# Optimization experiments

Measured on AMD Instinct MI355X. Metric: run time of the kernel, lower is better.

The kernel has to match this reference:

```python
import math
import jax, jax.numpy as jnp
import numpy as np

B, T, E = 1, 4096, 768
H, D = 12, 64
RA_WINDOW = 512
INIT_GATES = (2.2, 0.6, 0.1)


def setup_inputs() -> dict:
    key = jax.random.key(0)
    ks = jax.random.split(key, 6)
    x = jax.random.normal(ks[0], (B, T, E), dtype=jnp.float32)
    # Linear weights stored as [in, out] (math-equivalent to torch's x @ W.T)
    s = 1.0 / math.sqrt(E)
    Wq = jax.random.normal(ks[1], (E, H * D), dtype=jnp.float32) * s
    Wk = jax.random.normal(ks[2], (E, H * D), dtype=jnp.float32) * s
    Wv = jax.random.normal(ks[3], (E, H * D), dtype=jnp.float32) * s
    Wo = jax.random.normal(ks[4], (H * D, E), dtype=jnp.float32) * s
    gates = jnp.tile(jnp.asarray(INIT_GATES, dtype=jnp.float32)[None, :], (H, 1))  # [H,3]
    u = jax.random.normal(ks[5], (H, D), dtype=jnp.float32) * 0.02
    return {"x": x, "Wq": Wq, "Wk": Wk, "Wv": Wv, "Wo": Wo, "gates": gates, "u": u}


def reference(x, Wq, Wk, Wv, Wo, gates, u):
    # projections -> [B,H,T,D]
    def proj(W):
        return (x @ W).reshape(B, T, H, D).transpose(0, 2, 1, 3)
    Q, K, V = proj(Wq), proj(Wk), proj(Wv)

    S = jnp.einsum('bhtd,bhsd->bhts', Q, K) / math.sqrt(D)  # [B,H,T,T]

    w = jax.nn.softmax(gates, axis=-1)  # [H,3]
    w_std = w[:, 0][None, :, None, None]
    w_rec = w[:, 1][None, :, None, None]
    w_disc = w[:, 2][None, :, None, None]

    logits = w_std * S + w_rec * jnp.swapaxes(S, -2, -1)

    # discoverability column bias from K via per-head u
    d_raw = jnp.einsum('bhtd,hd->bht', K, u)
    d = d_raw - jnp.mean(d_raw, axis=-1, keepdims=True)
    logits = logits + w_disc * d[:, :, None, :]

    # causal banded mask
    idx = jnp.arange(T)
    mask = (idx[None, :] <= idx[:, None]) & (jnp.abs(idx[None, :] - idx[:, None]) <= RA_WINDOW)
    logits = jnp.where(mask[None, None, :, :], logits, -jnp.inf)

    attn = jax.nn.softmax(logits, axis=-1)
    ctx = jnp.einsum('bhts,bhsd->bhtd', attn, V)
    out = ctx.transpose(0, 2, 1, 3).reshape(B, T, H * D) @ Wo
    return (out, attn)
```

## Files before the change

kernel.cpp:

```cpp
#include <hip/hip_runtime.h>
#include <cstddef>

#define T_LEN 4096
#define EMB 768
#define NH 12
#define HD 64
#define WIN 512
#define PBW 640

#define GBM 128
#define GBN 128
#define GBK 16

__device__ __forceinline__ void gemm_128(const float* __restrict__ A,
                                         const float* __restrict__ B,
                                         float* __restrict__ C,
                                         int bm, int bn, int tid) {
    __shared__ float As[GBK][GBM + 4];
    __shared__ float Bs[GBK][GBN + 4];

    const int ty = (tid >> 4) << 2;
    const int tx = (tid & 15) << 2;

    const int ar = tid >> 1;
    const int ac = (tid & 1) << 3;
    const int br = tid >> 4;
    const int bc = (tid & 15) << 3;

    float acc[8][8] = {};

    float4 pa0 = *(const float4*)&A[(size_t)(bm + ar) * EMB + ac];
    float4 pa1 = *(const float4*)&A[(size_t)(bm + ar) * EMB + ac + 4];
    float4 pb0 = *(const float4*)&B[(size_t)br * EMB + bn + bc];
    float4 pb1 = *(const float4*)&B[(size_t)br * EMB + bn + bc + 4];

    for (int k0 = 0; k0 < EMB; k0 += GBK) {
        As[ac + 0][ar] = pa0.x; As[ac + 1][ar] = pa0.y; As[ac + 2][ar] = pa0.z; As[ac + 3][ar] = pa0.w;
        As[ac + 4][ar] = pa1.x; As[ac + 5][ar] = pa1.y; As[ac + 6][ar] = pa1.z; As[ac + 7][ar] = pa1.w;
        *(float4*)&Bs[br][bc]     = pb0;
        *(float4*)&Bs[br][bc + 4] = pb1;
        __syncthreads();
        if (k0 + GBK < EMB) {
            pa0 = *(const float4*)&A[(size_t)(bm + ar) * EMB + k0 + GBK + ac];
            pa1 = *(const float4*)&A[(size_t)(bm + ar) * EMB + k0 + GBK + ac + 4];
            pb0 = *(const float4*)&B[(size_t)(k0 + GBK + br) * EMB + bn + bc];
            pb1 = *(const float4*)&B[(size_t)(k0 + GBK + br) * EMB + bn + bc + 4];
        }
#pragma unroll
        for (int k = 0; k < GBK; ++k) {
            const float4 a0v = *(const float4*)&As[k][ty];
            const float4 a1v = *(const float4*)&As[k][ty + 64];
            const float4 b0v = *(const float4*)&Bs[k][tx];
            const float4 b1v = *(const float4*)&Bs[k][tx + 64];
            const float av[8] = {a0v.x, a0v.y, a0v.z, a0v.w, a1v.x, a1v.y, a1v.z, a1v.w};
            const float bv[8] = {b0v.x, b0v.y, b0v.z, b0v.w, b1v.x, b1v.y, b1v.z, b1v.w};
#pragma unroll
            for (int i = 0; i < 8; ++i)
#pragma unroll
                for (int j = 0; j < 8; ++j)
                    acc[i][j] += av[i] * bv[j];
        }
        __syncthreads();
    }
#pragma unroll
    for (int i = 0; i < 8; ++i) {
        const int r = bm + ty + ((i < 4) ? i : (60 + i));
        *(float4*)&C[(size_t)r * EMB + bn + tx]      = make_float4(acc[i][0], acc[i][1], acc[i][2], acc[i][3]);
        *(float4*)&C[(size_t)r * EMB + bn + tx + 64] = make_float4(acc[i][4], acc[i][5], acc[i][6], acc[i][7]);
    }
}

__global__ __launch_bounds__(256) void qkv_zero_kernel(const float* __restrict__ x,
                                                       const float* __restrict__ Wq,
                                                       const float* __restrict__ Wk,
                                                       const float* __restrict__ Wv,
                                                       float* __restrict__ Qb,
                                                       float* __restrict__ Kb,
                                                       float* __restrict__ Vb,
                                                       float* __restrict__ attn) {
    const int bid = blockIdx.x;
    const int tid = threadIdx.x;
    if (bid < 576) {
        const int z = bid / 192;
        const int r = bid % 192;
        const int bm = (r / 6) * GBM;
        const int bn = (r % 6) * GBN;
        const float* B = (z == 0) ? Wq : (z == 1) ? Wk : Wv;
        float* C = (z == 0) ? Qb : (z == 1) ? Kb : Vb;
        gemm_128(x, B, C, bm, bn, tid);
    } else {
        const int zb = bid - 576;
        const int rr0 = tid >> 6;
        const int ln = tid & 63;
        const float4 z4 = make_float4(0.f, 0.f, 0.f, 0.f);
        for (int k = 0; k < 4; ++k) {
            const int p = zb + 192 * k;
            const int h = p % NH;
            const int t0 = (p / NH) << 6;
            const int bl = (t0 >= 576) ? (t0 - 576) : 0;
            const int br = t0 + 64;
            for (int rr = rr0; rr < 64; rr += 4) {
                float* arow = attn + ((size_t)(h * T_LEN + t0 + rr)) * T_LEN;
                for (int c = ln << 2; c < bl; c += 256)
                    *(float4*)&arow[c] = z4;
                for (int c = br + (ln << 2); c < T_LEN; c += 256)
                    *(float4*)&arow[c] = z4;
            }
        }
    }
}

__global__ __launch_bounds__(256) void dbias_kernel(const float* __restrict__ K,
                                                    const float* __restrict__ u,
                                                    float* __restrict__ d_bias) {
    const int h = blockIdx.x;
    const int tid = threadIdx.x;
    __shared__ __align__(16) float us[HD];
    __shared__ float dr[T_LEN];
    __shared__ float red[256];
    if (tid < HD) us[tid] = u[h * HD + tid];
    __syncthreads();
    const float4* u4 = (const float4*)us;
    float lsum = 0.f;
    for (int t = tid; t < T_LEN; t += 256) {
        const float4* Kp = (const float4*)&K[(size_t)t * EMB + h * HD];
        float acc = 0.f;
#pragma unroll
        for (int i = 0; i < HD / 4; ++i) {
            float4 k4 = Kp[i];
            float4 uu = u4[i];
            acc += k4.x * uu.x + k4.y * uu.y + k4.z * uu.z + k4.w * uu.w;
        }
        dr[t] = acc;
        lsum += acc;
    }
    red[tid] = lsum;
    __syncthreads();
    for (int off = 128; off > 0; off >>= 1) {
        if (tid < off) red[tid] += red[tid + off];
        __syncthreads();
    }
    const float mean = red[0] * (1.0f / (float)T_LEN);
    __syncthreads();
    for (int t = tid; t < T_LEN; t += 256) {
        d_bias[h * T_LEN + t] = dr[t] - mean;
    }
}

__global__ __launch_bounds__(256) void attn_band_kernel(const float* __restrict__ Q,
                                                        const float* __restrict__ K,
                                                        const float* __restrict__ V,
                                                        const float* __restrict__ d_bias,
                                                        const float* __restrict__ gates,
                                                        float* __restrict__ Pb,
                                                        float* __restrict__ Fb,
                                                        float* __restrict__ ctx) {
    const int t0  = blockIdx.x << 6;
    const int h   = blockIdx.y;
    const int tid = threadIdx.x;
    const int cg  = tid & 15;
    const int tm  = (tid >> 4) << 2;
    const int tn4 = cg << 2;

    const int lm = tid >> 2;
    const int lk = (tid & 3) << 4;
    const int sr = tid >> 1;
    const int sc = (tid & 1) << 5;

    __shared__ __align__(16) float QT[64][68];
    __shared__ __align__(16) float KT[64][68];
    __shared__ __align__(16) float Bc[64][136];
    __shared__ float cmf[5][64];
    __shared__ float rmf[64], idvf[64];
    float* __restrict__ Bp = &Bc[0][0];

    const float g0 = gates[h * 3 + 0];
    const float g1 = gates[h * 3 + 1];
    const float g2 = gates[h * 3 + 2];
    const float gm = fmaxf(g0, fmaxf(g1, g2));
    const float e0 = __expf(g0 - gm), e1 = __expf(g1 - gm), e2 = __expf(g2 - gm);
    const float gi = 1.0f / (e0 + e1 + e2);
    const float w_std = e0 * gi * 0.125f;
    const float w_rec = e1 * gi * 0.125f;
    const float w_disc = e2 * gi;

    const int cp_start = (t0 >= 576) ? 0 : ((576 - t0) >> 7);
    int s0 = t0 - 576 + (cp_start << 7);

    float4 kr[8], qr[8];
    {
        int srow = s0 + sr; srow = srow < 0 ? 0 : srow;
        const float* Kp = K + (size_t)srow * EMB + h * HD + sc;
#pragma unroll
        for (int c = 0; c < 8; ++c) kr[c] = *(const float4*)(Kp + 4 * c);
    }

    {
        const float* Qp = Q + (size_t)(t0 + lm) * EMB + h * HD + lk;
        const float* Kp = K + (size_t)(t0 + lm) * EMB + h * HD + lk;
#pragma unroll
        for (int it = 0; it < 4; ++it) {
            float4 a = *(const float4*)(Qp + 4 * it);
            QT[lk + 4 * it + 0][lm] = a.x;
            QT[lk + 4 * it + 1][lm] = a.y;
            QT[lk + 4 * it + 2][lm] = a.z;
            QT[lk + 4 * it + 3][lm] = a.w;
            float4 b = *(const float4*)(Kp + 4 * it);
            KT[lk + 4 * it + 0][lm] = b.x;
            KT[lk + 4 * it + 1][lm] = b.y;
            KT[lk + 4 * it + 2][lm] = b.z;
            KT[lk + 4 * it + 3][lm] = b.w;
        }
    }

    float rm[4], rden[4], acc[4][4];
#pragma unroll
    for (int i = 0; i < 4; ++i) {
        rm[i] = -1e30f;
        rden[i] = 0.f;
#pragma unroll
        for (int j = 0; j < 4; ++j) acc[i][j] = 0.f;
    }

    for (int cp = cp_start; cp < 5; ++cp) {
        __syncthreads();
#pragma unroll
        for (int c = 0; c < 8; ++c) {
            Bc[sc + 4 * c + 0][sr] = kr[c].x;
            Bc[sc + 4 * c + 1][sr] = kr[c].y;
            Bc[sc + 4 * c + 2][sr] = kr[c].z;
            Bc[sc + 4 * c + 3][sr] = kr[c].w;
        }
        __syncthreads();

        {
            int srow = s0 + sr; srow = srow < 0 ? 0 : srow;
            const float* Qp = Q + (size_t)srow * EMB + h * HD + sc;
#pragma unroll
            for (int c = 0; c < 8; ++c) qr[c] = *(const float4*)(Qp + 4 * c);
        }

        float m1[4][8] = {};
#pragma unroll 8
        for (int k = 0; k < 64; ++k) {
            const float4 a4 = *(const float4*)&QT[k][tm];
            const float4 b0 = *(const float4*)&Bc[k][tn4];
            const float4 b1 = *(const float4*)&Bc[k][tn4 + 64];
            const float av[4] = {a4.x, a4.y, a4.z, a4.w};
            const float bv[8] = {b0.x, b0.y, b0.z, b0.w, b1.x, b1.y, b1.z, b1.w};
#pragma unroll
            for (int i = 0; i < 4; ++i)
#pragma unroll
                for (int j = 0; j < 8; ++j)
                    m1[i][j] += av[i] * bv[j];
        }
        __syncthreads();

#pragma unroll
        for (int c = 0; c < 8; ++c) {
            Bc[sc + 4 * c + 0][sr] = qr[c].x;
            Bc[sc + 4 * c + 1][sr] = qr[c].y;
            Bc[sc + 4 * c + 2][sr] = qr[c].z;
            Bc[sc + 4 * c + 3][sr] = qr[c].w;
        }
        __syncthreads();

        if (cp < 4) {
            int srow = s0 + 128 + sr; srow = srow < 0 ? 0 : srow;
            const float* Kp = K + (size_t)srow * EMB + h * HD + sc;
#pragma unroll
            for (int c = 0; c < 8; ++c) kr[c] = *(const float4*)(Kp + 4 * c);
        }

        float m2[4][8] = {};
#pragma unroll 8
        for (int k = 0; k < 64; ++k) {
            const float4 a4 = *(const float4*)&KT[k][tm];
            const float4 b0 = *(const float4*)&Bc[k][tn4];
            const float4 b1 = *(const float4*)&Bc[k][tn4 + 64];
            const float av[4] = {a4.x, a4.y, a4.z, a4.w};
            const float bv[8] = {b0.x, b0.y, b0.z, b0.w, b1.x, b1.y, b1.z, b1.w};
#pragma unroll
            for (int i = 0; i < 4; ++i)
#pragma unroll
                for (int j = 0; j < 8; ++j)
                    m2[i][j] += av[i] * bv[j];
        }

        const int i0 = s0 + tn4;
        const int i0c = i0 < 0 ? 0 : i0;
        const float4 db0 = *(const float4*)&d_bias[h * T_LEN + i0c];
        const float4 db1 = *(const float4*)&d_bias[h * T_LEN + s0 + 64 + tn4];
        const float dbv[8] = {db0.x, db0.y, db0.z, db0.w, db1.x, db1.y, db1.z, db1.w};
        float l[4][8];
#pragma unroll
        for (int i = 0; i < 4; ++i) {
            const int t = t0 + tm + i;
#pragma unroll
            for (int j = 0; j < 8; ++j) {
                const int s = s0 + ((j < 4) ? (tn4 + j) : (tn4 + j + 60));
                const float lv = w_std * m1[i][j] + w_rec * m2[i][j] + w_disc * dbv[j];
                const bool valid = (s >= 0) && (s <= t) && (s >= t - WIN);
                l[i][j] = valid ? lv : -1e30f;
            }
        }
#pragma unroll
        for (int i = 0; i < 4; ++i) {
            float cmx = fmaxf(fmaxf(fmaxf(l[i][0], l[i][1]), fmaxf(l[i][2], l[i][3])),
                              fmaxf(fmaxf(l[i][4], l[i][5]), fmaxf(l[i][6], l[i][7])));
#pragma unroll
            for (int off = 1; off < 16; off <<= 1) cmx = fmaxf(cmx, __shfl_xor(cmx, off));
            const float nm = fmaxf(rm[i], cmx);
            const float f = __expf(rm[i] - nm);
            float cs = 0.f;
#pragma unroll
            for (int j = 0; j < 8; ++j) {
                const float p = __expf(l[i][j] - nm);
                l[i][j] = p;
                cs += p;
            }
#pragma unroll
            for (int off = 1; off < 16; off <<= 1) cs += __shfl_xor(cs, off);
            rden[i] = rden[i] * f + cs;
            rm[i] = nm;
#pragma unroll
            for (int j = 0; j < 4; ++j) acc[i][j] *= f;
            if (cg == 0) cmf[cp][tm + i] = nm;
            float* prow = &Pb[((size_t)(h * T_LEN + t0 + tm + i)) * PBW + (cp << 7)];
            *(float4*)&prow[tn4]      = make_float4(l[i][0], l[i][1], l[i][2], l[i][3]);
            *(float4*)&prow[64 + tn4] = make_float4(l[i][4], l[i][5], l[i][6], l[i][7]);
        }
        __syncthreads();

#pragma unroll
        for (int j = 0; j < 4; ++j) {
            *(float4*)&Bp[(tn4 + j) * 68 + tm] =
                make_float4(l[0][j], l[1][j], l[2][j], l[3][j]);
            *(float4*)&Bp[(tn4 + j + 64) * 68 + tm] =
                make_float4(l[0][j + 4], l[1][j + 4], l[2][j + 4], l[3][j + 4]);
        }
        __syncthreads();

#pragma unroll 8
        for (int k = 0; k < 128; ++k) {
            const float4 av = *(const float4*)&Bp[k * 68 + tm];
            int vrow = s0 + k; vrow = vrow < 0 ? 0 : vrow;
            const float4 bv = *(const float4*)&V[(size_t)vrow * EMB + h * HD + tn4];
            acc[0][0] += av.x * bv.x; acc[0][1] += av.x * bv.y; acc[0][2] += av.x * bv.z; acc[0][3] += av.x * bv.w;
            acc[1][0] += av.y * bv.x; acc[1][1] += av.y * bv.y; acc[1][2] += av.y * bv.z; acc[1][3] += av.y * bv.w;
            acc[2][0] += av.z * bv.x; acc[2][1] += av.z * bv.y; acc[2][2] += av.z * bv.z; acc[2][3] += av.z * bv.w;
            acc[3][0] += av.w * bv.x; acc[3][1] += av.w * bv.y; acc[3][2] += av.w * bv.z; acc[3][3] += av.w * bv.w;
        }
        s0 += 128;
    }

    float idv[4];
#pragma unroll
    for (int i = 0; i < 4; ++i) {
        idv[i] = 1.0f / rden[i];
        *(float4*)&ctx[(size_t)(t0 + tm + i) * EMB + h * HD + tn4] =
            make_float4(acc[i][0] * idv[i], acc[i][1] * idv[i], acc[i][2] * idv[i], acc[i][3] * idv[i]);
    }
    if (cg == 0) {
#pragma unroll
        for (int i = 0; i < 4; ++i) {
            rmf[tm + i] = rm[i];
            idvf[tm + i] = idv[i];
        }
    }
    __syncthreads();
    for (int idx = tid; idx < 320; idx += 256) {
        const int c = idx >> 6, r = idx & 63;
        const float fct = (c >= cp_start) ? __expf(cmf[c][r] - rmf[r]) * idvf[r] : 0.f;
        Fb[((size_t)(h * T_LEN + t0 + r)) * 5 + c] = fct;
    }
}

__global__ __launch_bounds__(256) void wo_expand_kernel(const float* __restrict__ Cb,
                                                        const float* __restrict__ Wo,
                                                        float* __restrict__ out,
                                                        const float* __restrict__ Pb,
                                                        const float* __restrict__ Fb,
                                                        float* __restrict__ attn) {
    const int bid = blockIdx.x;
    const int tid = threadIdx.x;
    if (bid < 192) {
        const int bm = (bid / 6) * GBM;
        const int bn = (bid % 6) * GBN;
        gemm_128(Cb, Wo, out, bm, bn, tid);
    } else {
        const int e = bid - 192;
        const int h = e / 1024;
        const int t = ((e % 1024) << 2) + (tid >> 6);
        const int ln = tid & 63;
        const int base = (t & ~63) - 576;
        const int j_lo = (base < 0) ? -base : 0;
        const float* prow = Pb + ((size_t)(h * T_LEN + t)) * PBW;
        const float* frow = Fb + ((size_t)(h * T_LEN + t)) * 5;
        const float f0 = frow[0], f1 = frow[1], f2 = frow[2], f3 = frow[3], f4 = frow[4];
        float* arow = attn + ((size_t)(h * T_LEN + t)) * T_LEN;
        for (int j4 = j_lo + (ln << 2); j4 < PBW; j4 += 256) {
            const float4 p = *(const float4*)&prow[j4];
            const float ff = (j4 < 128) ? f0 : (j4 < 256) ? f1 : (j4 < 384) ? f2
                           : (j4 < 512) ? f3 : f4;
            *(float4*)&arow[base + j4] = make_float4(p.x * ff, p.y * ff, p.z * ff, p.w * ff);
        }
    }
}

extern "C" void kernel_launch(void* const* d_in, const int* in_sizes, int n_in,
                              void* d_out, int out_size, void* d_ws, size_t ws_size,
                              hipStream_t stream) {
    const float* x     = (const float*)d_in[0];
    const float* Wq    = (const float*)d_in[1];
    const float* Wk    = (const float*)d_in[2];
    const float* Wv    = (const float*)d_in[3];
    const float* Wo    = (const float*)d_in[4];
    const float* gates = (const float*)d_in[5];
    const float* u     = (const float*)d_in[6];

    float* out  = (float*)d_out;
    float* attn = out + (size_t)T_LEN * EMB;

    float* ws = (float*)d_ws;
    float* Qb = ws;
    float* Kb = Qb + (size_t)T_LEN * EMB;
    float* Vb = Kb + (size_t)T_LEN * EMB;
    float* Cb = Vb + (size_t)T_LEN * EMB;
    float* Db = Cb + (size_t)T_LEN * EMB;
    float* Pb = Db + (size_t)NH * T_LEN;
    float* Fb = Pb + (size_t)NH * T_LEN * PBW;

    qkv_zero_kernel<<<768, 256, 0, stream>>>(x, Wq, Wk, Wv, Qb, Kb, Vb, attn);
    dbias_kernel<<<NH, 256, 0, stream>>>(Kb, u, Db);

    attn_band_kernel<<<dim3(T_LEN / 64, NH), 256, 0, stream>>>(Qb, Kb, Vb, Db, gates,
                                                               Pb, Fb, Cb);

    wo_expand_kernel<<<192 + 12288, 256, 0, stream>>>(Cb, Wo, out, Pb, Fb, attn);
}
```

Measured before the change: 1.404 ms.

## Trim band to 576 columns and fold discoverability bias into QKV launch

The banded attention key range shrinks from 640 to 576 columns by handling the first 64-column chunk as a separate tile, so fewer partial scores are computed, stored and expanded. The discoverability bias is now computed directly from x and Wk·u inside the QKV/zero kernel as 12 extra blocks, which removes a separate launch and its dependency on K. The trade-offs are more code paths, a long serial dot product per thread in the bias blocks, and a possible tail from those 12 blocks.

```diff
diff --git a/kernel.cpp b/kernel.cpp
--- a/kernel.cpp
+++ b/kernel.cpp
@@ -6,7 +6,7 @@
 #define NH 12
 #define HD 64
 #define WIN 512
-#define PBW 640
+#define PBW 576
 
 #define GBM 128
 #define GBN 128
@@ -74,10 +74,12 @@
                                                        const float* __restrict__ Wq,
                                                        const float* __restrict__ Wk,
                                                        const float* __restrict__ Wv,
+                                                       const float* __restrict__ u,
                                                        float* __restrict__ Qb,
                                                        float* __restrict__ Kb,
                                                        float* __restrict__ Vb,
-                                                       float* __restrict__ attn) {
+                                                       float* __restrict__ attn,
+                                                       float* __restrict__ d_bias) {
     const int bid = blockIdx.x;
     const int tid = threadIdx.x;
     if (bid < 576) {
@@ -88,7 +90,7 @@
         const float* B = (z == 0) ? Wq : (z == 1) ? Wk : Wv;
         float* C = (z == 0) ? Qb : (z == 1) ? Kb : Vb;
         gemm_128(x, B, C, bm, bn, tid);
-    } else {
+    } else if (bid < 768) {
         const int zb = bid - 576;
         const int rr0 = tid >> 6;
         const int ln = tid & 63;
@@ -97,7 +99,7 @@
             const int p = zb + 192 * k;
             const int h = p % NH;
             const int t0 = (p / NH) << 6;
-            const int bl = (t0 >= 576) ? (t0 - 576) : 0;
+            const int bl = (t0 >= WIN) ? (t0 - WIN) : 0;
             const int br = t0 + 64;
             for (int rr = rr0; rr < 64; rr += 4) {
                 float* arow = attn + ((size_t)(h * T_LEN + t0 + rr)) * T_LEN;
@@ -107,43 +109,51 @@
                     *(float4*)&arow[c] = z4;
             }
         }
-    }
-}
-
-__global__ __launch_bounds__(256) void dbias_kernel(const float* __restrict__ K,
-                                                    const float* __restrict__ u,
-                                                    float* __restrict__ d_bias) {
-    const int h = blockIdx.x;
-    const int tid = threadIdx.x;
-    __shared__ __align__(16) float us[HD];
-    __shared__ float dr[T_LEN];
-    __shared__ float red[256];
-    if (tid < HD) us[tid] = u[h * HD + tid];
-    __syncthreads();
-    const float4* u4 = (const float4*)us;
-    float lsum = 0.f;
-    for (int t = tid; t < T_LEN; t += 256) {
-        const float4* Kp = (const float4*)&K[(size_t)t * EMB + h * HD];
-        float acc = 0.f;
-#pragma unroll
-        for (int i = 0; i < HD / 4; ++i) {
-            float4 k4 = Kp[i];
-            float4 uu = u4[i];
-            acc += k4.x * uu.x + k4.y * uu.y + k4.z * uu.z + k4.w * uu.w;
-        }
-        dr[t] = acc;
-        lsum += acc;
-    }
-    red[tid] = lsum;
-    __syncthreads();
-    for (int off = 128; off > 0; off >>= 1) {
-        if (tid < off) red[tid] += red[tid + off];
-        __syncthreads();
-    }
-    const float mean = red[0] * (1.0f / (float)T_LEN);
-    __syncthreads();
-    for (int t = tid; t < T_LEN; t += 256) {
-        d_bias[h * T_LEN + t] = dr[t] - mean;
+    } else {
+        const int h = bid - 768;
+        __shared__ __align__(16) float us[HD];
+        __shared__ __align__(16) float wku[EMB];
+        __shared__ float dr[T_LEN];
+        __shared__ float red[256];
+        if (tid < HD) us[tid] = u[h * HD + tid];
+        __syncthreads();
+        const float4* u4 = (const float4*)us;
+        for (int e = tid; e < EMB; e += 256) {
+            const float4* Wp = (const float4*)&Wk[(size_t)e * EMB + h * HD];
+            float a = 0.f;
+#pragma unroll
+            for (int i = 0; i < HD / 4; ++i) {
+                float4 w4 = Wp[i];
+                float4 uu = u4[i];
+                a += w4.x * uu.x + w4.y * uu.y + w4.z * uu.z + w4.w * uu.w;
+            }
+            wku[e] = a;
+        }
+        __syncthreads();
+        const float4* wk4 = (const float4*)wku;
+        float lsum = 0.f;
+        for (int t = tid; t < T_LEN; t += 256) {
+            const float4* xp = (const float4*)&x[(size_t)t * EMB];
+            float a = 0.f;
+#pragma unroll 8
+            for (int i = 0; i < EMB / 4; ++i) {
+                float4 xv = xp[i];
+                float4 wv = wk4[i];
+                a += xv.x * wv.x + xv.y * wv.y + xv.z * wv.z + xv.w * wv.w;
+            }
+            dr[t] = a;
+            lsum += a;
+        }
+        red[tid] = lsum;
+        __syncthreads();
+        for (int off = 128; off > 0; off >>= 1) {
+            if (tid < off) red[tid] += red[tid + off];
+            __syncthreads();
+        }
+        const float mean = red[0] * (1.0f / (float)T_LEN);
+        __syncthreads();
+        for (int t = tid; t < T_LEN; t += 256)
+            d_bias[h * T_LEN + t] = dr[t] - mean;
     }
 }
 
@@ -184,17 +194,6 @@
     const float w_rec = e1 * gi * 0.125f;
     const float w_disc = e2 * gi;
 
-    const int cp_start = (t0 >= 576) ? 0 : ((576 - t0) >> 7);
-    int s0 = t0 - 576 + (cp_start << 7);
-
-    float4 kr[8], qr[8];
-    {
-        int srow = s0 + sr; srow = srow < 0 ? 0 : srow;
-        const float* Kp = K + (size_t)srow * EMB + h * HD + sc;
-#pragma unroll
-        for (int c = 0; c < 8; ++c) kr[c] = *(const float4*)(Kp + 4 * c);
-    }
-
     {
         const float* Qp = Q + (size_t)(t0 + lm) * EMB + h * HD + lk;
         const float* Kp = K + (size_t)(t0 + lm) * EMB + h * HD + lk;
@@ -222,7 +221,124 @@
         for (int j = 0; j < 4; ++j) acc[i][j] = 0.f;
     }
 
-    for (int cp = cp_start; cp < 5; ++cp) {
+    if (t0 >= WIN) {
+        const int s0 = t0 - WIN;
+        {
+            const float* Kp = K + (size_t)(s0 + lm) * EMB + h * HD + lk;
+#pragma unroll
+            for (int it = 0; it < 4; ++it) {
+                float4 b = *(const float4*)(Kp + 4 * it);
+                Bc[lk + 4 * it + 0][lm] = b.x;
+                Bc[lk + 4 * it + 1][lm] = b.y;
+                Bc[lk + 4 * it + 2][lm] = b.z;
+                Bc[lk + 4 * it + 3][lm] = b.w;
+            }
+        }
+        __syncthreads();
+        float m1c[4][4] = {};
+#pragma unroll 8
+        for (int k = 0; k < 64; ++k) {
+            const float4 a4 = *(const float4*)&QT[k][tm];
+            const float4 b0 = *(const float4*)&Bc[k][tn4];
+            const float av[4] = {a4.x, a4.y, a4.z, a4.w};
+            const float bv[4] = {b0.x, b0.y, b0.z, b0.w};
+#pragma unroll
+            for (int i = 0; i < 4; ++i)
+#pragma unroll
+                for (int j = 0; j < 4; ++j)
+                    m1c[i][j] += av[i] * bv[j];
+        }
+        __syncthreads();
+        {
+            const float* Qp = Q + (size_t)(s0 + lm) * EMB + h * HD + lk;
+#pragma unroll
+            for (int it = 0; it < 4; ++it) {
+                float4 b = *(const float4*)(Qp + 4 * it);
+                Bc[lk + 4 * it + 0][lm] = b.x;
+                Bc[lk + 4 * it + 1][lm] = b.y;
+                Bc[lk + 4 * it + 2][lm] = b.z;
+                Bc[lk + 4 * it + 3][lm] = b.w;
+            }
+        }
+        __syncthreads();
+        float m2c[4][4] = {};
+#pragma unroll 8
+        for (int k = 0; k < 64; ++k) {
+            const float4 a4 = *(const float4*)&KT[k][tm];
+            const float4 b0 = *(const float4*)&Bc[k][tn4];
+            const float av[4] = {a4.x, a4.y, a4.z, a4.w};
+            const float bv[4] = {b0.x, b0.y, b0.z, b0.w};
+#pragma unroll
+            for (int i = 0; i < 4; ++i)
+#pragma unroll
+                for (int j = 0; j < 4; ++j)
+                    m2c[i][j] += av[i] * bv[j];
+        }
+        const float4 db = *(const float4*)&d_bias[h * T_LEN + s0 + tn4];
+        const float dbv[4] = {db.x, db.y, db.z, db.w};
+        float lc[4][4];
+#pragma unroll
+        for (int i = 0; i < 4; ++i) {
+            const int t = t0 + tm + i;
+#pragma unroll
+            for (int j = 0; j < 4; ++j) {
+                const int s = s0 + tn4 + j;
+                const float lv = w_std * m1c[i][j] + w_rec * m2c[i][j] + w_disc * dbv[j];
+                lc[i][j] = (s >= t - WIN) ? lv : -1e30f;
+            }
+        }
+#pragma unroll
+        for (int i = 0; i < 4; ++i) {
+            float cmx = fmaxf(fmaxf(lc[i][0], lc[i][1]), fmaxf(lc[i][2], lc[i][3]));
+#pragma unroll
+            for (int off = 1; off < 16; off <<= 1) cmx = fmaxf(cmx, __shfl_xor(cmx, off));
+            const float nm = fmaxf(rm[i], cmx);
+            const float f = __expf(rm[i] - nm);
+            float cs = 0.f;
+#pragma unroll
+            for (int j = 0; j < 4; ++j) {
+                const float p = __expf(lc[i][j] - nm);
+                lc[i][j] = p;
+                cs += p;
+            }
+#pragma unroll
+            for (int off = 1; off < 16; off <<= 1) cs += __shfl_xor(cs, off);
+            rden[i] = rden[i] * f + cs;
+            rm[i] = nm;
+#pragma unroll
+            for (int j = 0; j < 4; ++j) acc[i][j] *= f;
+            if (cg == 0) cmf[0][tm + i] = nm;
+            float* prow = &Pb[((size_t)(h * T_LEN + t0 + tm + i)) * PBW];
+            *(float4*)&prow[tn4] = make_float4(lc[i][0], lc[i][1], lc[i][2], lc[i][3]);
+        }
+        __syncthreads();
+#pragma unroll
+        for (int j = 0; j < 4; ++j)
+            *(float4*)&Bc[tn4 + j][tm] = make_float4(lc[0][j], lc[1][j], lc[2][j], lc[3][j]);
+        __syncthreads();
+#pragma unroll 8
+        for (int k = 0; k < 64; ++k) {
+            const float4 av = *(const float4*)&Bc[k][tm];
+            const float4 bv = *(const float4*)&V[(size_t)(s0 + k) * EMB + h * HD + tn4];
+            acc[0][0] += av.x * bv.x; acc[0][1] += av.x * bv.y; acc[0][2] += av.x * bv.z; acc[0][3] += av.x * bv.w;
+            acc[1][0] += av.y * bv.x; acc[1][1] += av.y * bv.y; acc[1][2] += av.y * bv.z; acc[1][3] += av.y * bv.w;
+            acc[2][0] += av.z * bv.x; acc[2][1] += av.z * bv.y; acc[2][2] += av.z * bv.z; acc[2][3] += av.z * bv.w;
+            acc[3][0] += av.w * bv.x; acc[3][1] += av.w * bv.y; acc[3][2] += av.w * bv.z; acc[3][3] += av.w * bv.w;
+        }
+    }
+
+    const int p_start = (t0 > 320) ? 0 : (((320 - t0) >> 7) + 1);
+    int s0 = t0 - 448 + (p_start << 7);
+
+    float4 kr[8], qr[8];
+    {
+        int srow = s0 + sr; srow = srow < 0 ? 0 : srow;
+        const float* Kp = K + (size_t)srow * EMB + h * HD + sc;
+#pragma unroll
+        for (int c = 0; c < 8; ++c) kr[c] = *(const float4*)(Kp + 4 * c);
+    }
+
+    for (int cp = p_start; cp < 4; ++cp) {
         __syncthreads();
 #pragma unroll
         for (int c = 0; c < 8; ++c) {
@@ -265,7 +381,7 @@
         }
         __syncthreads();
 
-        if (cp < 4) {
+        if (cp < 3) {
             int srow = s0 + 128 + sr; srow = srow < 0 ? 0 : srow;
             const float* Kp = K + (size_t)srow * EMB + h * HD + sc;
 #pragma unroll
@@ -325,9 +441,10 @@
             rm[i] = nm;
 #pragma unroll
             for (int j = 0; j < 4; ++j) acc[i][j] *= f;
-            if (cg == 0) cmf[cp][tm + i] = nm;
-            float* prow = &Pb[((size_t)(h * T_LEN + t0 + tm + i)) * PBW + (cp << 7)];
-            *(float4*)&prow[tn4]      = make_float4(l[i][0], l[i][1], l[i][2], l[i][3]);
+            if (cg == 0) cmf[1 + cp][tm + i] = nm;
+            float* prow = &Pb[((size_t)(h * T_LEN + t0 + tm + i)) * PBW + 64 + (cp << 7)];
+            if (s0 >= 0)
+                *(float4*)&prow[tn4] = make_float4(l[i][0], l[i][1], l[i][2], l[i][3]);
             *(float4*)&prow[64 + tn4] = make_float4(l[i][4], l[i][5], l[i][6], l[i][7]);
         }
         __syncthreads();
@@ -371,7 +488,8 @@
     __syncthreads();
     for (int idx = tid; idx < 320; idx += 256) {
         const int c = idx >> 6, r = idx & 63;
-        const float fct = (c >= cp_start) ? __expf(cmf[c][r] - rmf[r]) * idvf[r] : 0.f;
+        const bool live = (c == 0) ? (t0 >= WIN) : ((c - 1) >= p_start);
+        const float fct = live ? __expf(cmf[c][r] - rmf[r]) * idvf[r] : 0.f;
         Fb[((size_t)(h * T_LEN + t0 + r)) * 5 + c] = fct;
     }
 }
@@ -393,7 +511,7 @@
         const int h = e / 1024;
         const int t = ((e % 1024) << 2) + (tid >> 6);
         const int ln = tid & 63;
-        const int base = (t & ~63) - 576;
+        const int base = (t & ~63) - WIN;
         const int j_lo = (base < 0) ? -base : 0;
         const float* prow = Pb + ((size_t)(h * T_LEN + t)) * PBW;
         const float* frow = Fb + ((size_t)(h * T_LEN + t)) * 5;
@@ -401,8 +519,8 @@
         float* arow = attn + ((size_t)(h * T_LEN + t)) * T_LEN;
         for (int j4 = j_lo + (ln << 2); j4 < PBW; j4 += 256) {
             const float4 p = *(const float4*)&prow[j4];
-            const float ff = (j4 < 128) ? f0 : (j4 < 256) ? f1 : (j4 < 384) ? f2
-                           : (j4 < 512) ? f3 : f4;
+            const float ff = (j4 < 64) ? f0 : (j4 < 192) ? f1 : (j4 < 320) ? f2
+                           : (j4 < 448) ? f3 : f4;
             *(float4*)&arow[base + j4] = make_float4(p.x * ff, p.y * ff, p.z * ff, p.w * ff);
         }
     }
@@ -431,8 +549,7 @@
     float* Pb = Db + (size_t)NH * T_LEN;
     float* Fb = Pb + (size_t)NH * T_LEN * PBW;
 
-    qkv_zero_kernel<<<768, 256, 0, stream>>>(x, Wq, Wk, Wv, Qb, Kb, Vb, attn);
-    dbias_kernel<<<NH, 256, 0, stream>>>(Kb, u, Db);
+    qkv_zero_kernel<<<780, 256, 0, stream>>>(x, Wq, Wk, Wv, u, Qb, Kb, Vb, attn, Db);
 
     attn_band_kernel<<<dim3(T_LEN / 64, NH), 256, 0, stream>>>(Qb, Kb, Vb, Db, gates,
                                                                Pb, Fb, Cb);
```

Measured after the change: 1.626 ms. 15.8% more time.
